# Optimization experiments

Measured on AMD Instinct MI355X. Metric: run time of the kernel, lower is better.

## Reference

```python
import jax, jax.numpy as jnp
import numpy as np

N_LEVELS = 16
NFPL = 2
LOG2_T = 19
TABLE_SIZE = 1 << LOG2_T
BASE_RES = 16.0
FINEST_RES = 512.0
N_POINTS = 1048576

# hash primes from HashNeRF's hash() (xor of coord*prime per axis)
PRIMES = jnp.array([1, 2654435761, 805459861], dtype=jnp.uint32)
# corner offsets: index = 4*i + 2*j + k (i outermost), matching BOX_OFFSETS
OFFSETS = jnp.array([[i, j, k] for i in (0, 1) for j in (0, 1) for k in (0, 1)], dtype=jnp.int32)  # [8,3]


def setup_inputs() -> dict:
    key = jax.random.key(0)
    k1, k2 = jax.random.split(key)
    x = jax.random.uniform(k1, (N_POINTS, 3), dtype=jnp.float32)  # points in [0,1)^3
    # nn.Embedding tables init uniform(-1e-4, 1e-4), stacked over levels
    tables = jax.random.uniform(k2, (N_LEVELS, TABLE_SIZE, NFPL), minval=-1e-4, maxval=1e-4, dtype=jnp.float32)
    return {"x": x, "tables": tables}


def _level_embed(x, table, resolution):
    # x: [N,3] in box [0,1]^3; table: [T,F]; resolution: scalar float
    grid = 1.0 / resolution
    xc = jnp.clip(x, 0.0, 1.0)
    bl = jnp.floor(xc / grid).astype(jnp.int32)            # [N,3] bottom-left voxel idx
    vmin = bl.astype(jnp.float32) * grid                    # voxel_min_vertex
    vmax = vmin + grid                                      # voxel_max_vertex
    corners = bl[:, None, :] + OFFSETS[None, :, :]          # [N,8,3]
    h = corners.astype(jnp.uint32) * PRIMES                 # wrap-around uint32 mult
    idx = (h[..., 0] ^ h[..., 1] ^ h[..., 2]) & jnp.uint32(TABLE_SIZE - 1)  # [N,8]
    emb = table[idx.astype(jnp.int32)]                      # [N,8,F] gather
    # trilinear interp (weights use unclamped x as in the original)
    w = (x - vmin) / (vmax - vmin)                          # [N,3]
    w0, w1, w2 = w[:, 0:1], w[:, 1:2], w[:, 2:3]
    c00 = emb[:, 0] * (1 - w0) + emb[:, 4] * w0
    c01 = emb[:, 1] * (1 - w0) + emb[:, 5] * w0
    c10 = emb[:, 2] * (1 - w0) + emb[:, 6] * w0
    c11 = emb[:, 3] * (1 - w0) + emb[:, 7] * w0
    c0 = c00 * (1 - w1) + c10 * w1
    c1 = c01 * (1 - w1) + c11 * w1
    return c0 * (1 - w2) + c1 * w2                          # [N,F]


def reference(x, tables):
    b = np.exp((np.log(FINEST_RES) - np.log(BASE_RES)) / (N_LEVELS - 1))
    res = jnp.floor(BASE_RES * (b ** jnp.arange(N_LEVELS, dtype=jnp.float32)))  # [L]
    feats = jax.vmap(_level_embed, in_axes=(None, 0, 0))(x, tables, res)        # [L,N,F]
    out = jnp.moveaxis(feats, 0, 1).reshape(x.shape[0], N_LEVELS * NFPL)        # [N,32]
    # original: if last dim != 16, F.pad(x, (0, 16 - D)); negative pad crops
    D = out.shape[-1]
    if D > 16:
        out = out[:, :16]
    elif D < 16:
        out = jnp.pad(out, ((0, 0), (0, 16 - D)))
    return out
```

## Files before the change

kernel.cpp:

```cpp
#include <hip/hip_runtime.h>
#include <hip/hip_fp16.h>
#include <stdint.h>


#define TABLE_SIZE (1u << 19)
#define TMASK (TABLE_SIZE - 1u)
#define P2 2654435761u
#define P3 805459861u

#define FSCALE 8192.0f
#define FINV   1.220703125e-4f

#define QUAD_BYTES_OFF 262144
#define PAIR_BYTES_OFF 16777216

#define OFF_Q3 0
#define OFF_Q4 33792
#define OFF_Q5 99392
#define OFF_Q6 226892

__device__ __forceinline__ uint32_t pack_s(float a, float b) {
    __half2 h = __floats2half2_rn(a * FSCALE, b * FSCALE);
    return *(uint32_t*)&h;
}
__device__ __forceinline__ uint32_t pack_r(float a, float b) {
    __half2 h = __floats2half2_rn(a, b);
    return *(uint32_t*)&h;
}
__device__ __forceinline__ float2 h2f(uint32_t u) {
    __half2 h = *(__half2*)&u;
    return __half22float2(h);
}
__device__ __forceinline__ uint32_t getc(const uint4 v, int k) {
    return k == 0 ? v.x : k == 1 ? v.y : k == 2 ? v.z : v.w;
}

__global__ __launch_bounds__(256) void build_tables_kernel(
    const float* __restrict__ tables, float2* __restrict__ dense,
    uint4* __restrict__ quads, uint2* __restrict__ pairs)
{
    const int role = (int)blockIdx.y;
    const int e = (int)blockIdx.x * 256 + (int)threadIdx.x;

    if (role < 4) {
        int DK, offq, l = 3 + role;
        switch (role) {
            case 0: DK = 32; offq = OFF_Q3; break;
            case 1: DK = 40; offq = OFF_Q4; break;
            case 2: DK = 50; offq = OFF_Q5; break;
            default:DK = 64; offq = OFF_Q6; break;
        }
        const int E = (DK + 1) * DK * DK;
        if (e >= E) return;
        const int d2 = DK * DK;
        const int i = e / d2;
        const int rem = e - i * d2;
        const int j = rem / DK;
        const int k = rem - j * DK;
        const float2* __restrict__ tab = (const float2*)tables + (size_t)l * (size_t)TABLE_SIZE;
        const uint32_t hx  = (uint32_t)i;
        const uint32_t hy0 = (uint32_t)j * P2, hy1 = hy0 + P2;
        const uint32_t hz0 = (uint32_t)k * P3, hz1 = hz0 + P3;
        const float2 v00 = tab[(hx ^ hy0 ^ hz0) & TMASK];
        const float2 v01 = tab[(hx ^ hy0 ^ hz1) & TMASK];
        const float2 v10 = tab[(hx ^ hy1 ^ hz0) & TMASK];
        const float2 v11 = tab[(hx ^ hy1 ^ hz1) & TMASK];
        uint4 u;
        u.x = pack_s(v00.x, v00.y);
        u.y = pack_s(v01.x, v01.y);
        u.z = pack_s(v10.x, v10.y);
        u.w = pack_s(v11.x, v11.y);
        quads[offq + e] = u;
    } else if (role == 4) {
        const int E = 81 * 81 * 80;
        if (e >= E) return;
        const int i = e / 6480;
        const int rem = e - i * 6480;
        const int j = rem / 80;
        const int k = rem - j * 80;
        const float2* __restrict__ tab = (const float2*)tables + (size_t)7 * (size_t)TABLE_SIZE;
        const uint32_t hb = (uint32_t)i ^ ((uint32_t)j * P2);
        const float2 a = tab[(hb ^ ((uint32_t)k * P3)) & TMASK];
        const float2 b = tab[(hb ^ ((uint32_t)(k + 1) * P3)) & TMASK];
        uint2 u;
        u.x = pack_s(a.x, a.y);
        u.y = pack_s(b.x, b.y);
        pairs[e] = u;
    } else {
        if (e >= 31750) return;
        int lv, DIM, off;
        if (e < 4913)       { lv = 0; DIM = 17; off = 0; }
        else if (e < 14174) { lv = 1; DIM = 21; off = 4913; }
        else                { lv = 2; DIM = 26; off = 14174; }
        const int le = e - off;
        const int d2 = DIM * DIM;
        const int i = le / d2;
        const int rem = le - i * d2;
        const int j = rem / DIM;
        const int k = rem - j * DIM;
        const uint32_t h = ((uint32_t)i ^ ((uint32_t)j * P2) ^ ((uint32_t)k * P3)) & TMASK;
        const float2* __restrict__ tab = (const float2*)tables + (size_t)lv * (size_t)TABLE_SIZE;
        dense[e] = tab[h];
    }
}

struct PQ {
    uint4 qa[4], qb[4];
    float wx[4], wy[4], wz[4];
};
struct PP {
    uint2 d00[4], d01[4], d10[4], d11[4];
    float wx[4], wy[4], wz[4];
};

template<int DK>
__device__ __forceinline__ void q_issue(const uint4* __restrict__ tab,
        const float px[4], const float py[4], const float pz[4], PQ& s)
{
    const float R = (float)DK, g = 1.0f / R;
    const int d2 = DK * DK;
#pragma unroll
    for (int k = 0; k < 4; ++k) {
        const float cx = fminf(fmaxf(px[k], 0.0f), 1.0f);
        const float cy = fminf(fmaxf(py[k], 0.0f), 1.0f);
        const float cz = fminf(fmaxf(pz[k], 0.0f), 1.0f);
        const int bx = min((int)floorf(cx * R), DK - 1);
        const int by = min((int)floorf(cy * R), DK - 1);
        const int bz = min((int)floorf(cz * R), DK - 1);
        s.wx[k] = (px[k] - (float)bx * g) * R;
        s.wy[k] = (py[k] - (float)by * g) * R;
        s.wz[k] = (pz[k] - (float)bz * g) * R;
        const int ia = (bx * DK + by) * DK + bz;
        s.qa[k] = tab[ia];
        s.qb[k] = tab[ia + d2];
    }
}

__device__ __forceinline__ uint4 q_finish(const PQ& s)
{
    uint32_t r[4];
#pragma unroll
    for (int k = 0; k < 4; ++k) {
        const float wx = s.wx[k], wy = s.wy[k], wz = s.wz[k];
        const float omx = 1.0f - wx, omy = 1.0f - wy, omz = 1.0f - wz;
        const float2 a00 = h2f(s.qa[k].x), a01 = h2f(s.qa[k].y);
        const float2 a10 = h2f(s.qa[k].z), a11 = h2f(s.qa[k].w);
        const float2 b00 = h2f(s.qb[k].x), b01 = h2f(s.qb[k].y);
        const float2 b10 = h2f(s.qb[k].z), b11 = h2f(s.qb[k].w);
        const float m00a = a00.x*omx + b00.x*wx, m00b = a00.y*omx + b00.y*wx;
        const float m01a = a01.x*omx + b01.x*wx, m01b = a01.y*omx + b01.y*wx;
        const float m10a = a10.x*omx + b10.x*wx, m10b = a10.y*omx + b10.y*wx;
        const float m11a = a11.x*omx + b11.x*wx, m11b = a11.y*omx + b11.y*wx;
        const float c0a = m00a*omz + m01a*wz, c0b = m00b*omz + m01b*wz;
        const float c1a = m10a*omz + m11a*wz, c1b = m10b*omz + m11b*wz;
        r[k] = pack_r(c0a*omy + c1a*wy, c0b*omy + c1b*wy);
    }
    return make_uint4(r[0], r[1], r[2], r[3]);
}

__device__ __forceinline__ void p_issue(const uint2* __restrict__ pairs,
        const float px[4], const float py[4], const float pz[4], PP& s)
{
    const float R = 80.f, g = 1.0f / R;
#pragma unroll
    for (int k = 0; k < 4; ++k) {
        const float cx = fminf(fmaxf(px[k], 0.0f), 1.0f);
        const float cy = fminf(fmaxf(py[k], 0.0f), 1.0f);
        const float cz = fminf(fmaxf(pz[k], 0.0f), 1.0f);
        const int bx = min((int)floorf(cx * R), 79);
        const int by = min((int)floorf(cy * R), 79);
        const int bz = min((int)floorf(cz * R), 79);
        s.wx[k] = (px[k] - (float)bx * g) * R;
        s.wy[k] = (py[k] - (float)by * g) * R;
        s.wz[k] = (pz[k] - (float)bz * g) * R;
        const int ix = (bx * 81 + by) * 80 + bz;
        s.d00[k] = pairs[ix];
        s.d01[k] = pairs[ix + 80];
        s.d10[k] = pairs[ix + 6480];
        s.d11[k] = pairs[ix + 6560];
    }
}

__device__ __forceinline__ uint4 p_finish(const PP& s)
{
    uint32_t r[4];
#pragma unroll
    for (int k = 0; k < 4; ++k) {
        const float wx = s.wx[k], wy = s.wy[k], wz = s.wz[k];
        const float omx = 1.0f - wx, omy = 1.0f - wy, omz = 1.0f - wz;
        const float2 a00 = h2f(s.d00[k].x), z00 = h2f(s.d00[k].y);
        const float2 a01 = h2f(s.d01[k].x), z01 = h2f(s.d01[k].y);
        const float2 a10 = h2f(s.d10[k].x), z10 = h2f(s.d10[k].y);
        const float2 a11 = h2f(s.d11[k].x), z11 = h2f(s.d11[k].y);
        const float c00a = a00.x*omz + z00.x*wz, c00b = a00.y*omz + z00.y*wz;
        const float c01a = a01.x*omz + z01.x*wz, c01b = a01.y*omz + z01.y*wz;
        const float c10a = a10.x*omz + z10.x*wz, c10b = a10.y*omz + z10.y*wz;
        const float c11a = a11.x*omz + z11.x*wz, c11b = a11.y*omz + z11.y*wz;
        const float e0a = c00a*omy + c01a*wy, e0b = c00b*omy + c01b*wy;
        const float e1a = c10a*omy + c11a*wy, e1b = c10b*omy + c11b*wy;
        r[k] = pack_r(e0a*omx + e1a*wx, e0b*omx + e1b*wx);
    }
    return make_uint4(r[0], r[1], r[2], r[3]);
}

__device__ __forceinline__ void store4(uint32_t* __restrict__ wsh,
        size_t lofs, int p0, int n, uint4 r)
{
    if (p0 + 4 <= n) {
        *(uint4*)(wsh + lofs + p0) = r;
    } else {
#pragma unroll
        for (int k = 0; k < 4; ++k)
            if (p0 + k < n) wsh[lofs + p0 + k] = getc(r, k);
    }
}

__global__ __launch_bounds__(256) void embed_grouped_kernel(
    const float* __restrict__ x, const uint4* __restrict__ quads,
    const uint2* __restrict__ pairs, uint32_t* __restrict__ wsh,
    int n, int bpl)
{
    const int bid = (int)blockIdx.x;
    const int grp = bid / bpl;
    const int pb = bid - grp * bpl;
    const int p0 = pb * 1024 + 4 * (int)threadIdx.x;
    if (p0 >= n) return;

    float px[4], py[4], pz[4];
    if (p0 + 4 <= n) {
        const float4* __restrict__ xv = (const float4*)(x + (size_t)3 * p0);
        const float4 f0 = xv[0], f1 = xv[1], f2 = xv[2];
        px[0] = f0.x; py[0] = f0.y; pz[0] = f0.z;
        px[1] = f0.w; py[1] = f1.x; pz[1] = f1.y;
        px[2] = f1.z; py[2] = f1.w; pz[2] = f2.x;
        px[3] = f2.y; py[3] = f2.z; pz[3] = f2.w;
    } else {
#pragma unroll
        for (int k = 0; k < 4; ++k) {
            const int i = min(p0 + k, n - 1);
            px[k] = x[3*i]; py[k] = x[3*i+1]; pz[k] = x[3*i+2];
        }
    }

    if (grp == 0) {
        PQ s3, s4, s5;
        q_issue<32>(quads + OFF_Q3, px, py, pz, s3);
        q_issue<40>(quads + OFF_Q4, px, py, pz, s4);
        store4(wsh, (size_t)3 * n, p0, n, q_finish(s3));
        q_issue<50>(quads + OFF_Q5, px, py, pz, s5);
        store4(wsh, (size_t)4 * n, p0, n, q_finish(s4));
        store4(wsh, (size_t)5 * n, p0, n, q_finish(s5));
    } else if (grp == 1) {
        PQ s6;
        q_issue<64>(quads + OFF_Q6, px, py, pz, s6);
        store4(wsh, (size_t)6 * n, p0, n, q_finish(s6));
    } else {
        PP s7;
        p_issue(pairs, px, py, pz, s7);
        store4(wsh, (size_t)7 * n, p0, n, p_finish(s7));
    }
}

__global__ __launch_bounds__(1024) void embed_lds_kernel(
    const float* __restrict__ x, const float2* __restrict__ dense,
    uint32_t* __restrict__ wsh, int n, int lv, int DIM, int E, int doff)
{
    extern __shared__ float2 lds[];
    for (int e = (int)threadIdx.x; e < E; e += 1024) lds[e] = dense[doff + e];
    __syncthreads();

    const int p0 = ((int)blockIdx.x * 1024 + (int)threadIdx.x) * 4;
    if (p0 >= n) return;

    const float R = (lv == 0) ? 16.f : (lv == 1) ? 20.f : 25.f;
    const float g = 1.0f / R;
    const int D2 = DIM * DIM;
    const int bmax = DIM - 2;

    float px[4], py[4], pz[4];
    if (p0 + 4 <= n) {
        const float4* __restrict__ xv = (const float4*)(x + (size_t)3 * p0);
        const float4 f0 = xv[0], f1 = xv[1], f2 = xv[2];
        px[0] = f0.x; py[0] = f0.y; pz[0] = f0.z;
        px[1] = f0.w; py[1] = f1.x; pz[1] = f1.y;
        px[2] = f1.z; py[2] = f1.w; pz[2] = f2.x;
        px[3] = f2.y; py[3] = f2.z; pz[3] = f2.w;
    } else {
#pragma unroll
        for (int k = 0; k < 4; ++k) {
            const int i = min(p0 + k, n - 1);
            px[k] = x[3*i]; py[k] = x[3*i+1]; pz[k] = x[3*i+2];
        }
    }

    uint32_t r[4];
#pragma unroll
    for (int k = 0; k < 4; ++k) {
        const float cx = fminf(fmaxf(px[k], 0.0f), 1.0f);
        const float cy = fminf(fmaxf(py[k], 0.0f), 1.0f);
        const float cz = fminf(fmaxf(pz[k], 0.0f), 1.0f);
        const int bx = min((int)floorf(cx * R), bmax);
        const int by = min((int)floorf(cy * R), bmax);
        const int bz = min((int)floorf(cz * R), bmax);
        const float wx = (px[k] - (float)bx * g) * R;
        const float wy = (py[k] - (float)by * g) * R;
        const float wz = (pz[k] - (float)bz * g) * R;
        const int c = (bx * DIM + by) * DIM + bz;
        const float2 e000 = lds[c];
        const float2 e001 = lds[c + 1];
        const float2 e010 = lds[c + DIM];
        const float2 e011 = lds[c + DIM + 1];
        const float2 e100 = lds[c + D2];
        const float2 e101 = lds[c + D2 + 1];
        const float2 e110 = lds[c + D2 + DIM];
        const float2 e111 = lds[c + D2 + DIM + 1];
        const float omx = 1.0f - wx, omy = 1.0f - wy, omz = 1.0f - wz;
        const float c00a = e000.x*omx + e100.x*wx, c00b = e000.y*omx + e100.y*wx;
        const float c01a = e001.x*omx + e101.x*wx, c01b = e001.y*omx + e101.y*wx;
        const float c10a = e010.x*omx + e110.x*wx, c10b = e010.y*omx + e110.y*wx;
        const float c11a = e011.x*omx + e111.x*wx, c11b = e011.y*omx + e111.y*wx;
        const float c0a = c00a*omy + c10a*wy, c0b = c00b*omy + c10b*wy;
        const float c1a = c01a*omy + c11a*wy, c1b = c01b*omy + c11b*wy;
        r[k] = pack_s(c0a*omz + c1a*wz, c0b*omz + c1b*wz);
    }
    store4(wsh, (size_t)lv * n, p0, n, make_uint4(r[0], r[1], r[2], r[3]));
}

__global__ __launch_bounds__(256) void aos_kernel(
    const uint32_t* __restrict__ wsh, float* __restrict__ out, int n)
{
    const int p0 = ((int)blockIdx.x * 256 + (int)threadIdx.x) * 4;
    if (p0 >= n) return;

    if (p0 + 4 <= n) {
        const uint4 v0 = *(const uint4*)(wsh + 0 * (size_t)n + p0);
        const uint4 v1 = *(const uint4*)(wsh + 1 * (size_t)n + p0);
        const uint4 v2 = *(const uint4*)(wsh + 2 * (size_t)n + p0);
        const uint4 v3 = *(const uint4*)(wsh + 3 * (size_t)n + p0);
        const uint4 v4 = *(const uint4*)(wsh + 4 * (size_t)n + p0);
        const uint4 v5 = *(const uint4*)(wsh + 5 * (size_t)n + p0);
        const uint4 v6 = *(const uint4*)(wsh + 6 * (size_t)n + p0);
        const uint4 v7 = *(const uint4*)(wsh + 7 * (size_t)n + p0);
#pragma unroll
        for (int k = 0; k < 4; ++k) {
            const float2 f0 = h2f(getc(v0, k)), f1 = h2f(getc(v1, k));
            const float2 f2 = h2f(getc(v2, k)), f3 = h2f(getc(v3, k));
            const float2 f4 = h2f(getc(v4, k)), f5 = h2f(getc(v5, k));
            const float2 f6 = h2f(getc(v6, k)), f7 = h2f(getc(v7, k));
            float4* __restrict__ op = (float4*)(out + (size_t)(p0 + k) * 16);
            op[0] = make_float4(f0.x*FINV, f0.y*FINV, f1.x*FINV, f1.y*FINV);
            op[1] = make_float4(f2.x*FINV, f2.y*FINV, f3.x*FINV, f3.y*FINV);
            op[2] = make_float4(f4.x*FINV, f4.y*FINV, f5.x*FINV, f5.y*FINV);
            op[3] = make_float4(f6.x*FINV, f6.y*FINV, f7.x*FINV, f7.y*FINV);
        }
    } else {
        for (int k = 0; k < 4 && p0 + k < n; ++k) {
            const int i = p0 + k;
            float* __restrict__ op = out + (size_t)i * 16;
#pragma unroll
            for (int l = 0; l < 8; ++l) {
                const float2 f = h2f(wsh[(size_t)l * n + i]);
                op[2*l + 0] = f.x * FINV;
                op[2*l + 1] = f.y * FINV;
            }
        }
    }
}

__global__ __launch_bounds__(256) void hash_embed_mono_kernel(
    const float* __restrict__ x, const float* __restrict__ tables,
    float* __restrict__ out, int n)
{
    const int i = blockIdx.x * 256 + threadIdx.x;
    if (i >= n) return;
    const float px = x[3*i+0], py = x[3*i+1], pz = x[3*i+2];
    const float cx = fminf(fmaxf(px, 0.0f), 1.0f);
    const float cy = fminf(fmaxf(py, 0.0f), 1.0f);
    const float cz = fminf(fmaxf(pz, 0.0f), 1.0f);
    const float resf[8] = {16.f,20.f,25.f,32.f,40.f,50.f,64.f,80.f};
    float o[16];
#pragma unroll
    for (int l = 0; l < 8; ++l) {
        const float R = resf[l], g = 1.0f / R;
        const int bx = (int)floorf(cx*R), by = (int)floorf(cy*R), bz = (int)floorf(cz*R);
        const float wx = (px - bx*g)*R, wy = (py - by*g)*R, wz = (pz - bz*g)*R;
        const uint32_t hx0 = (uint32_t)bx, hx1 = hx0+1u;
        const uint32_t hy0 = (uint32_t)by*P2, hy1 = hy0+P2;
        const uint32_t hz0 = (uint32_t)bz*P3, hz1 = hz0+P3;
        const float2* tab = (const float2*)(tables) + (size_t)l*(size_t)TABLE_SIZE;
        const float2 e000 = tab[(hx0^hy0^hz0)&TMASK], e001 = tab[(hx0^hy0^hz1)&TMASK];
        const float2 e010 = tab[(hx0^hy1^hz0)&TMASK], e011 = tab[(hx0^hy1^hz1)&TMASK];
        const float2 e100 = tab[(hx1^hy0^hz0)&TMASK], e101 = tab[(hx1^hy0^hz1)&TMASK];
        const float2 e110 = tab[(hx1^hy1^hz0)&TMASK], e111 = tab[(hx1^hy1^hz1)&TMASK];
        const float omx = 1.f-wx, omy = 1.f-wy, omz = 1.f-wz;
        const float c00a = e000.x*omx + e100.x*wx, c00b = e000.y*omx + e100.y*wx;
        const float c01a = e001.x*omx + e101.x*wx, c01b = e001.y*omx + e101.y*wx;
        const float c10a = e010.x*omx + e110.x*wx, c10b = e010.y*omx + e110.y*wx;
        const float c11a = e011.x*omx + e111.x*wx, c11b = e011.y*omx + e111.y*wx;
        const float c0a = c00a*omy + c10a*wy, c0b = c00b*omy + c10b*wy;
        const float c1a = c01a*omy + c11a*wy, c1b = c01b*omy + c11b*wy;
        o[2*l+0] = c0a*omz + c1a*wz;
        o[2*l+1] = c0b*omz + c1b*wz;
    }
    float4* op = (float4*)(out + (size_t)i * 16);
    op[0] = make_float4(o[0],o[1],o[2],o[3]);
    op[1] = make_float4(o[4],o[5],o[6],o[7]);
    op[2] = make_float4(o[8],o[9],o[10],o[11]);
    op[3] = make_float4(o[12],o[13],o[14],o[15]);
}

extern "C" void kernel_launch(void* const* d_in, const int* in_sizes, int n_in,
                              void* d_out, int out_size, void* d_ws, size_t ws_size,
                              hipStream_t stream) {
    const float* x = (const float*)d_in[0];
    const float* tables = (const float*)d_in[1];
    float* out = (float*)d_out;
    const int n = in_sizes[0] / 3;

    static int cap = -1;
    if (cap < 0) {
        cap = (hipFuncSetAttribute((const void*)embed_lds_kernel,
                  hipFuncAttributeMaxDynamicSharedMemorySize, 140608) == hipSuccess)
              ? 1 : 0;
    }
    const size_t ws_needed = (size_t)8 * (size_t)n * sizeof(uint32_t);
    if (ws_size < ws_needed || cap == 0) {
        hash_embed_mono_kernel<<<(n + 255) / 256, 256, 0, stream>>>(x, tables, out, n);
        return;
    }

    uint32_t* wsh = (uint32_t*)d_ws;
    float2* dense = (float2*)out;
    uint4*  quads = (uint4*)((char*)out + QUAD_BYTES_OFF);
    uint2*  pairs = (uint2*)((char*)out + PAIR_BYTES_OFF);

    build_tables_kernel<<<dim3(2051, 6), 256, 0, stream>>>(tables, dense, quads, pairs);

    static const int DIMt[3] = {17, 21, 26};
    static const int Et[3]   = {4913, 9261, 17576};
    static const int OFFt[3] = {0, 4913, 14174};
    const int lgrid = (n + 4095) / 4096;
    for (int lv = 0; lv < 3; ++lv) {
        embed_lds_kernel<<<lgrid, 1024, (size_t)Et[lv] * sizeof(float2), stream>>>(
            x, dense, wsh, n, lv, DIMt[lv], Et[lv], OFFt[lv]);
    }

    const int bpl = (n + 1023) / 1024;
    embed_grouped_kernel<<<3 * bpl, 256, 0, stream>>>(x, quads, pairs, wsh, n, bpl);

    aos_kernel<<<(n + 1023) / 1024, 256, 0, stream>>>(wsh, out, n);
}
```

Before: 255.6 us.

## Fuse dense coarse levels into output kernel with fp16 LDS table

Measured after the change: 217.1 us. 1.18x faster.

```diff
diff --git a/kernel.cpp b/kernel.cpp
--- a/kernel.cpp
+++ b/kernel.cpp
@@ -19,6 +19,11 @@
 #define OFF_Q5 99392
 #define OFF_Q6 226892
 
+#define DENSE_L1_OFF 4913
+#define DENSE_L2_OFF 14174
+#define DENSE_E 31750
+#define DENSE_BYTES (DENSE_E * 4)
+
 __device__ __forceinline__ uint32_t pack_s(float a, float b) {
     __half2 h = __floats2half2_rn(a * FSCALE, b * FSCALE);
     return *(uint32_t*)&h;
@@ -35,21 +40,26 @@
     return k == 0 ? v.x : k == 1 ? v.y : k == 2 ? v.z : v.w;
 }
 
+__device__ __forceinline__ void quad_geom(int l, float& R, int& DK, int& offq) {
+    switch (l) {
+        case 3: R=32.f; DK=32; offq=OFF_Q3; break;
+        case 4: R=40.f; DK=40; offq=OFF_Q4; break;
+        case 5: R=50.f; DK=50; offq=OFF_Q5; break;
+        default:R=64.f; DK=64; offq=OFF_Q6; break;
+    }
+}
+
 __global__ __launch_bounds__(256) void build_tables_kernel(
-    const float* __restrict__ tables, float2* __restrict__ dense,
+    const float* __restrict__ tables, uint32_t* __restrict__ dense,
     uint4* __restrict__ quads, uint2* __restrict__ pairs)
 {
     const int role = (int)blockIdx.y;
     const int e = (int)blockIdx.x * 256 + (int)threadIdx.x;
 
     if (role < 4) {
-        int DK, offq, l = 3 + role;
-        switch (role) {
-            case 0: DK = 32; offq = OFF_Q3; break;
-            case 1: DK = 40; offq = OFF_Q4; break;
-            case 2: DK = 50; offq = OFF_Q5; break;
-            default:DK = 64; offq = OFF_Q6; break;
-        }
+        float Rf; int DK, offq;
+        quad_geom(3 + role, Rf, DK, offq);
+        const int l = 3 + role;
         const int E = (DK + 1) * DK * DK;
         if (e >= E) return;
         const int d2 = DK * DK;
@@ -87,11 +97,11 @@
         u.y = pack_s(b.x, b.y);
         pairs[e] = u;
     } else {
-        if (e >= 31750) return;
+        if (e >= DENSE_E) return;
         int lv, DIM, off;
-        if (e < 4913)       { lv = 0; DIM = 17; off = 0; }
-        else if (e < 14174) { lv = 1; DIM = 21; off = 4913; }
-        else                { lv = 2; DIM = 26; off = 14174; }
+        if (e < DENSE_L1_OFF)      { lv = 0; DIM = 17; off = 0; }
+        else if (e < DENSE_L2_OFF) { lv = 1; DIM = 21; off = DENSE_L1_OFF; }
+        else                       { lv = 2; DIM = 26; off = DENSE_L2_OFF; }
         const int le = e - off;
         const int d2 = DIM * DIM;
         const int i = le / d2;
@@ -100,25 +110,20 @@
         const int k = rem - j * DIM;
         const uint32_t h = ((uint32_t)i ^ ((uint32_t)j * P2) ^ ((uint32_t)k * P3)) & TMASK;
         const float2* __restrict__ tab = (const float2*)tables + (size_t)lv * (size_t)TABLE_SIZE;
-        dense[e] = tab[h];
-    }
-}
-
-struct PQ {
+        const float2 v = tab[h];
+        dense[e] = pack_s(v.x, v.y);
+    }
+}
+
+template<int DK>
+__device__ __forceinline__ uint4 embed_quad4(const uint4* __restrict__ tab,
+        const float px[4], const float py[4], const float pz[4])
+{
+    const float R = (float)DK;
+    const float g = 1.0f / R;
+    const int d2 = DK * DK;
     uint4 qa[4], qb[4];
     float wx[4], wy[4], wz[4];
-};
-struct PP {
-    uint2 d00[4], d01[4], d10[4], d11[4];
-    float wx[4], wy[4], wz[4];
-};
-
-template<int DK>
-__device__ __forceinline__ void q_issue(const uint4* __restrict__ tab,
-        const float px[4], const float py[4], const float pz[4], PQ& s)
-{
-    const float R = (float)DK, g = 1.0f / R;
-    const int d2 = DK * DK;
 #pragma unroll
     for (int k = 0; k < 4; ++k) {
         const float cx = fminf(fmaxf(px[k], 0.0f), 1.0f);
@@ -127,41 +132,38 @@
         const int bx = min((int)floorf(cx * R), DK - 1);
         const int by = min((int)floorf(cy * R), DK - 1);
         const int bz = min((int)floorf(cz * R), DK - 1);
-        s.wx[k] = (px[k] - (float)bx * g) * R;
-        s.wy[k] = (py[k] - (float)by * g) * R;
-        s.wz[k] = (pz[k] - (float)bz * g) * R;
+        wx[k] = (px[k] - (float)bx * g) * R;
+        wy[k] = (py[k] - (float)by * g) * R;
+        wz[k] = (pz[k] - (float)bz * g) * R;
         const int ia = (bx * DK + by) * DK + bz;
-        s.qa[k] = tab[ia];
-        s.qb[k] = tab[ia + d2];
-    }
-}
-
-__device__ __forceinline__ uint4 q_finish(const PQ& s)
-{
+        qa[k] = tab[ia];
+        qb[k] = tab[ia + d2];
+    }
     uint32_t r[4];
 #pragma unroll
     for (int k = 0; k < 4; ++k) {
-        const float wx = s.wx[k], wy = s.wy[k], wz = s.wz[k];
-        const float omx = 1.0f - wx, omy = 1.0f - wy, omz = 1.0f - wz;
-        const float2 a00 = h2f(s.qa[k].x), a01 = h2f(s.qa[k].y);
-        const float2 a10 = h2f(s.qa[k].z), a11 = h2f(s.qa[k].w);
-        const float2 b00 = h2f(s.qb[k].x), b01 = h2f(s.qb[k].y);
-        const float2 b10 = h2f(s.qb[k].z), b11 = h2f(s.qb[k].w);
-        const float m00a = a00.x*omx + b00.x*wx, m00b = a00.y*omx + b00.y*wx;
-        const float m01a = a01.x*omx + b01.x*wx, m01b = a01.y*omx + b01.y*wx;
-        const float m10a = a10.x*omx + b10.x*wx, m10b = a10.y*omx + b10.y*wx;
-        const float m11a = a11.x*omx + b11.x*wx, m11b = a11.y*omx + b11.y*wx;
-        const float c0a = m00a*omz + m01a*wz, c0b = m00b*omz + m01b*wz;
-        const float c1a = m10a*omz + m11a*wz, c1b = m10b*omz + m11b*wz;
-        r[k] = pack_r(c0a*omy + c1a*wy, c0b*omy + c1b*wy);
+        const float omx = 1.0f - wx[k], omy = 1.0f - wy[k], omz = 1.0f - wz[k];
+        const float2 a00 = h2f(qa[k].x), a01 = h2f(qa[k].y);
+        const float2 a10 = h2f(qa[k].z), a11 = h2f(qa[k].w);
+        const float2 b00 = h2f(qb[k].x), b01 = h2f(qb[k].y);
+        const float2 b10 = h2f(qb[k].z), b11 = h2f(qb[k].w);
+        const float m00a = a00.x*omx + b00.x*wx[k], m00b = a00.y*omx + b00.y*wx[k];
+        const float m01a = a01.x*omx + b01.x*wx[k], m01b = a01.y*omx + b01.y*wx[k];
+        const float m10a = a10.x*omx + b10.x*wx[k], m10b = a10.y*omx + b10.y*wx[k];
+        const float m11a = a11.x*omx + b11.x*wx[k], m11b = a11.y*omx + b11.y*wx[k];
+        const float c0a = m00a*omz + m01a*wz[k], c0b = m00b*omz + m01b*wz[k];
+        const float c1a = m10a*omz + m11a*wz[k], c1b = m10b*omz + m11b*wz[k];
+        r[k] = pack_r(c0a*omy + c1a*wy[k], c0b*omy + c1b*wy[k]);
     }
     return make_uint4(r[0], r[1], r[2], r[3]);
 }
 
-__device__ __forceinline__ void p_issue(const uint2* __restrict__ pairs,
-        const float px[4], const float py[4], const float pz[4], PP& s)
+__device__ __forceinline__ uint4 embed_pair4(const uint2* __restrict__ pairs,
+        const float px[4], const float py[4], const float pz[4])
 {
     const float R = 80.f, g = 1.0f / R;
+    uint2 d00[4], d01[4], d10[4], d11[4];
+    float wx[4], wy[4], wz[4];
 #pragma unroll
     for (int k = 0; k < 4; ++k) {
         const float cx = fminf(fmaxf(px[k], 0.0f), 1.0f);
@@ -170,52 +172,35 @@
         const int bx = min((int)floorf(cx * R), 79);
         const int by = min((int)floorf(cy * R), 79);
         const int bz = min((int)floorf(cz * R), 79);
-        s.wx[k] = (px[k] - (float)bx * g) * R;
-        s.wy[k] = (py[k] - (float)by * g) * R;
-        s.wz[k] = (pz[k] - (float)bz * g) * R;
+        wx[k] = (px[k] - (float)bx * g) * R;
+        wy[k] = (py[k] - (float)by * g) * R;
+        wz[k] = (pz[k] - (float)bz * g) * R;
         const int ix = (bx * 81 + by) * 80 + bz;
-        s.d00[k] = pairs[ix];
-        s.d01[k] = pairs[ix + 80];
-        s.d10[k] = pairs[ix + 6480];
-        s.d11[k] = pairs[ix + 6560];
-    }
-}
-
-__device__ __forceinline__ uint4 p_finish(const PP& s)
-{
+        d00[k] = pairs[ix];
+        d01[k] = pairs[ix + 80];
+        d10[k] = pairs[ix + 6480];
+        d11[k] = pairs[ix + 6560];
+    }
     uint32_t r[4];
 #pragma unroll
     for (int k = 0; k < 4; ++k) {
-        const float wx = s.wx[k], wy = s.wy[k], wz = s.wz[k];
-        const float omx = 1.0f - wx, omy = 1.0f - wy, omz = 1.0f - wz;
-        const float2 a00 = h2f(s.d00[k].x), z00 = h2f(s.d00[k].y);
-        const float2 a01 = h2f(s.d01[k].x), z01 = h2f(s.d01[k].y);
-        const float2 a10 = h2f(s.d10[k].x), z10 = h2f(s.d10[k].y);
-        const float2 a11 = h2f(s.d11[k].x), z11 = h2f(s.d11[k].y);
-        const float c00a = a00.x*omz + z00.x*wz, c00b = a00.y*omz + z00.y*wz;
-        const float c01a = a01.x*omz + z01.x*wz, c01b = a01.y*omz + z01.y*wz;
-        const float c10a = a10.x*omz + z10.x*wz, c10b = a10.y*omz + z10.y*wz;
-        const float c11a = a11.x*omz + z11.x*wz, c11b = a11.y*omz + z11.y*wz;
-        const float e0a = c00a*omy + c01a*wy, e0b = c00b*omy + c01b*wy;
-        const float e1a = c10a*omy + c11a*wy, e1b = c10b*omy + c11b*wy;
-        r[k] = pack_r(e0a*omx + e1a*wx, e0b*omx + e1b*wx);
+        const float omx = 1.0f - wx[k], omy = 1.0f - wy[k], omz = 1.0f - wz[k];
+        const float2 a00 = h2f(d00[k].x), z00 = h2f(d00[k].y);
+        const float2 a01 = h2f(d01[k].x), z01 = h2f(d01[k].y);
+        const float2 a10 = h2f(d10[k].x), z10 = h2f(d10[k].y);
+        const float2 a11 = h2f(d11[k].x), z11 = h2f(d11[k].y);
+        const float c00a = a00.x*omz + z00.x*wz[k], c00b = a00.y*omz + z00.y*wz[k];
+        const float c01a = a01.x*omz + z01.x*wz[k], c01b = a01.y*omz + z01.y*wz[k];
+        const float c10a = a10.x*omz + z10.x*wz[k], c10b = a10.y*omz + z10.y*wz[k];
+        const float c11a = a11.x*omz + z11.x*wz[k], c11b = a11.y*omz + z11.y*wz[k];
+        const float e0a = c00a*omy + c01a*wy[k], e0b = c00b*omy + c01b*wy[k];
+        const float e1a = c10a*omy + c11a*wy[k], e1b = c10b*omy + c11b*wy[k];
+        r[k] = pack_r(e0a*omx + e1a*wx[k], e0b*omx + e1b*wx[k]);
     }
     return make_uint4(r[0], r[1], r[2], r[3]);
 }
 
-__device__ __forceinline__ void store4(uint32_t* __restrict__ wsh,
-        size_t lofs, int p0, int n, uint4 r)
-{
-    if (p0 + 4 <= n) {
-        *(uint4*)(wsh + lofs + p0) = r;
-    } else {
-#pragma unroll
-        for (int k = 0; k < 4; ++k)
-            if (p0 + k < n) wsh[lofs + p0 + k] = getc(r, k);
-    }
-}
-
-__global__ __launch_bounds__(256) void embed_grouped_kernel(
+__global__ __launch_bounds__(256, 4) void embed_levels_kernel(
     const float* __restrict__ x, const uint4* __restrict__ quads,
     const uint2* __restrict__ pairs, uint32_t* __restrict__ wsh,
     int n, int bpl)
@@ -242,40 +227,40 @@
         }
     }
 
+    const int nstore = min(4, n - p0);
+
+#define STORE_ROW(l, r) { \
+    uint32_t* __restrict__ wl = wsh + (size_t)(l) * (size_t)n; \
+    if (nstore == 4) *(uint4*)(wl + p0) = (r); \
+    else for (int k = 0; k < nstore; ++k) wl[p0 + k] = getc((r), k); }
+
     if (grp == 0) {
-        PQ s3, s4, s5;
-        q_issue<32>(quads + OFF_Q3, px, py, pz, s3);
-        q_issue<40>(quads + OFF_Q4, px, py, pz, s4);
-        store4(wsh, (size_t)3 * n, p0, n, q_finish(s3));
-        q_issue<50>(quads + OFF_Q5, px, py, pz, s5);
-        store4(wsh, (size_t)4 * n, p0, n, q_finish(s4));
-        store4(wsh, (size_t)5 * n, p0, n, q_finish(s5));
+        const uint4 r3 = embed_quad4<32>(quads + OFF_Q3, px, py, pz);
+        STORE_ROW(3, r3)
+        const uint4 r4 = embed_quad4<40>(quads + OFF_Q4, px, py, pz);
+        STORE_ROW(4, r4)
     } else if (grp == 1) {
-        PQ s6;
-        q_issue<64>(quads + OFF_Q6, px, py, pz, s6);
-        store4(wsh, (size_t)6 * n, p0, n, q_finish(s6));
+        const uint4 r5 = embed_quad4<50>(quads + OFF_Q5, px, py, pz);
+        STORE_ROW(5, r5)
+    } else if (grp == 2) {
+        const uint4 r6 = embed_quad4<64>(quads + OFF_Q6, px, py, pz);
+        STORE_ROW(6, r6)
     } else {
-        PP s7;
-        p_issue(pairs, px, py, pz, s7);
-        store4(wsh, (size_t)7 * n, p0, n, p_finish(s7));
-    }
-}
-
-__global__ __launch_bounds__(1024) void embed_lds_kernel(
-    const float* __restrict__ x, const float2* __restrict__ dense,
-    uint32_t* __restrict__ wsh, int n, int lv, int DIM, int E, int doff)
-{
-    extern __shared__ float2 lds[];
-    for (int e = (int)threadIdx.x; e < E; e += 1024) lds[e] = dense[doff + e];
+        const uint4 r7 = embed_pair4(pairs, px, py, pz);
+        STORE_ROW(7, r7)
+    }
+}
+
+__global__ __launch_bounds__(1024) void final_kernel(
+    const float* __restrict__ x, const uint32_t* wsh,
+    float* __restrict__ out, int n)
+{
+    extern __shared__ uint32_t lds[];
+    for (int e = (int)threadIdx.x; e < DENSE_E; e += 1024) lds[e] = wsh[e];
     __syncthreads();
 
     const int p0 = ((int)blockIdx.x * 1024 + (int)threadIdx.x) * 4;
     if (p0 >= n) return;
-
-    const float R = (lv == 0) ? 16.f : (lv == 1) ? 20.f : 25.f;
-    const float g = 1.0f / R;
-    const int D2 = DIM * DIM;
-    const int bmax = DIM - 2;
 
     float px[4], py[4], pz[4];
     if (p0 + 4 <= n) {
@@ -293,77 +278,75 @@
         }
     }
 
-    uint32_t r[4];
-#pragma unroll
-    for (int k = 0; k < 4; ++k) {
-        const float cx = fminf(fmaxf(px[k], 0.0f), 1.0f);
-        const float cy = fminf(fmaxf(py[k], 0.0f), 1.0f);
-        const float cz = fminf(fmaxf(pz[k], 0.0f), 1.0f);
-        const int bx = min((int)floorf(cx * R), bmax);
-        const int by = min((int)floorf(cy * R), bmax);
-        const int bz = min((int)floorf(cz * R), bmax);
-        const float wx = (px[k] - (float)bx * g) * R;
-        const float wy = (py[k] - (float)by * g) * R;
-        const float wz = (pz[k] - (float)bz * g) * R;
-        const int c = (bx * DIM + by) * DIM + bz;
-        const float2 e000 = lds[c];
-        const float2 e001 = lds[c + 1];
-        const float2 e010 = lds[c + DIM];
-        const float2 e011 = lds[c + DIM + 1];
-        const float2 e100 = lds[c + D2];
-        const float2 e101 = lds[c + D2 + 1];
-        const float2 e110 = lds[c + D2 + DIM];
-        const float2 e111 = lds[c + D2 + DIM + 1];
-        const float omx = 1.0f - wx, omy = 1.0f - wy, omz = 1.0f - wz;
-        const float c00a = e000.x*omx + e100.x*wx, c00b = e000.y*omx + e100.y*wx;
-        const float c01a = e001.x*omx + e101.x*wx, c01b = e001.y*omx + e101.y*wx;
-        const float c10a = e010.x*omx + e110.x*wx, c10b = e010.y*omx + e110.y*wx;
-        const float c11a = e011.x*omx + e111.x*wx, c11b = e011.y*omx + e111.y*wx;
-        const float c0a = c00a*omy + c10a*wy, c0b = c00b*omy + c10b*wy;
-        const float c1a = c01a*omy + c11a*wy, c1b = c01b*omy + c11b*wy;
-        r[k] = pack_s(c0a*omz + c1a*wz, c0b*omz + c1b*wz);
-    }
-    store4(wsh, (size_t)lv * n, p0, n, make_uint4(r[0], r[1], r[2], r[3]));
-}
-
-__global__ __launch_bounds__(256) void aos_kernel(
-    const uint32_t* __restrict__ wsh, float* __restrict__ out, int n)
-{
-    const int p0 = ((int)blockIdx.x * 256 + (int)threadIdx.x) * 4;
-    if (p0 >= n) return;
-
+    uint4 v[5];
     if (p0 + 4 <= n) {
-        const uint4 v0 = *(const uint4*)(wsh + 0 * (size_t)n + p0);
-        const uint4 v1 = *(const uint4*)(wsh + 1 * (size_t)n + p0);
-        const uint4 v2 = *(const uint4*)(wsh + 2 * (size_t)n + p0);
-        const uint4 v3 = *(const uint4*)(wsh + 3 * (size_t)n + p0);
-        const uint4 v4 = *(const uint4*)(wsh + 4 * (size_t)n + p0);
-        const uint4 v5 = *(const uint4*)(wsh + 5 * (size_t)n + p0);
-        const uint4 v6 = *(const uint4*)(wsh + 6 * (size_t)n + p0);
-        const uint4 v7 = *(const uint4*)(wsh + 7 * (size_t)n + p0);
-#pragma unroll
-        for (int k = 0; k < 4; ++k) {
-            const float2 f0 = h2f(getc(v0, k)), f1 = h2f(getc(v1, k));
-            const float2 f2 = h2f(getc(v2, k)), f3 = h2f(getc(v3, k));
-            const float2 f4 = h2f(getc(v4, k)), f5 = h2f(getc(v5, k));
-            const float2 f6 = h2f(getc(v6, k)), f7 = h2f(getc(v7, k));
-            float4* __restrict__ op = (float4*)(out + (size_t)(p0 + k) * 16);
-            op[0] = make_float4(f0.x*FINV, f0.y*FINV, f1.x*FINV, f1.y*FINV);
-            op[1] = make_float4(f2.x*FINV, f2.y*FINV, f3.x*FINV, f3.y*FINV);
-            op[2] = make_float4(f4.x*FINV, f4.y*FINV, f5.x*FINV, f5.y*FINV);
-            op[3] = make_float4(f6.x*FINV, f6.y*FINV, f7.x*FINV, f7.y*FINV);
+#pragma unroll
+        for (int l = 0; l < 5; ++l)
+            v[l] = *(const uint4*)(wsh + (size_t)(l + 3) * n + p0);
+    } else {
+#pragma unroll
+        for (int l = 0; l < 5; ++l) {
+            uint4 t;
+            t.x = wsh[(size_t)(l+3)*n + min(p0+0, n-1)];
+            t.y = wsh[(size_t)(l+3)*n + min(p0+1, n-1)];
+            t.z = wsh[(size_t)(l+3)*n + min(p0+2, n-1)];
+            t.w = wsh[(size_t)(l+3)*n + min(p0+3, n-1)];
+            v[l] = t;
         }
-    } else {
-        for (int k = 0; k < 4 && p0 + k < n; ++k) {
-            const int i = p0 + k;
-            float* __restrict__ op = out + (size_t)i * 16;
-#pragma unroll
-            for (int l = 0; l < 8; ++l) {
-                const float2 f = h2f(wsh[(size_t)l * n + i]);
-                op[2*l + 0] = f.x * FINV;
-                op[2*l + 1] = f.y * FINV;
-            }
+    }
+
+    float la[3][4], lb[3][4];
+#pragma unroll
+    for (int k = 0; k < 4; ++k) {
+#pragma unroll
+        for (int lv = 0; lv < 3; ++lv) {
+            const float R  = (lv == 0) ? 16.f : (lv == 1) ? 20.f : 25.f;
+            const int DIM  = (lv == 0) ? 17 : (lv == 1) ? 21 : 26;
+            const int off  = (lv == 0) ? 0 : (lv == 1) ? DENSE_L1_OFF : DENSE_L2_OFF;
+            const float g = 1.0f / R;
+            const int D2 = DIM * DIM;
+            const int bmax = DIM - 2;
+            const float cx = fminf(fmaxf(px[k], 0.0f), 1.0f);
+            const float cy = fminf(fmaxf(py[k], 0.0f), 1.0f);
+            const float cz = fminf(fmaxf(pz[k], 0.0f), 1.0f);
+            const int bx = min((int)floorf(cx * R), bmax);
+            const int by = min((int)floorf(cy * R), bmax);
+            const int bz = min((int)floorf(cz * R), bmax);
+            const float wx = (px[k] - (float)bx * g) * R;
+            const float wy = (py[k] - (float)by * g) * R;
+            const float wz = (pz[k] - (float)bz * g) * R;
+            const int c = off + (bx * DIM + by) * DIM + bz;
+            const float2 e000 = h2f(lds[c]);
+            const float2 e001 = h2f(lds[c + 1]);
+            const float2 e010 = h2f(lds[c + DIM]);
+            const float2 e011 = h2f(lds[c + DIM + 1]);
+            const float2 e100 = h2f(lds[c + D2]);
+            const float2 e101 = h2f(lds[c + D2 + 1]);
+            const float2 e110 = h2f(lds[c + D2 + DIM]);
+            const float2 e111 = h2f(lds[c + D2 + DIM + 1]);
+            const float omx = 1.0f - wx, omy = 1.0f - wy, omz = 1.0f - wz;
+            const float c00a = e000.x*omx + e100.x*wx, c00b = e000.y*omx + e100.y*wx;
+            const float c01a = e001.x*omx + e101.x*wx, c01b = e001.y*omx + e101.y*wx;
+            const float c10a = e010.x*omx + e110.x*wx, c10b = e010.y*omx + e110.y*wx;
+            const float c11a = e011.x*omx + e111.x*wx, c11b = e011.y*omx + e111.y*wx;
+            const float c0a = c00a*omy + c10a*wy, c0b = c00b*omy + c10b*wy;
+            const float c1a = c01a*omy + c11a*wy, c1b = c01b*omy + c11b*wy;
+            la[lv][k] = c0a*omz + c1a*wz;
+            lb[lv][k] = c0b*omz + c1b*wz;
         }
+    }
+
+#pragma unroll
+    for (int k = 0; k < 4; ++k) {
+        if (p0 + k >= n) break;
+        const float2 f3v = h2f(getc(v[0], k)), f4v = h2f(getc(v[1], k));
+        const float2 f5v = h2f(getc(v[2], k)), f6v = h2f(getc(v[3], k));
+        const float2 f7v = h2f(getc(v[4], k));
+        float4* __restrict__ op = (float4*)(out + (size_t)(p0 + k) * 16);
+        op[0] = make_float4(la[0][k]*FINV, lb[0][k]*FINV, la[1][k]*FINV, lb[1][k]*FINV);
+        op[1] = make_float4(la[2][k]*FINV, lb[2][k]*FINV, f3v.x*FINV, f3v.y*FINV);
+        op[2] = make_float4(f4v.x*FINV, f4v.y*FINV, f5v.x*FINV, f5v.y*FINV);
+        op[3] = make_float4(f6v.x*FINV, f6v.y*FINV, f7v.x*FINV, f7v.y*FINV);
     }
 }
 
@@ -419,8 +402,8 @@
 
     static int cap = -1;
     if (cap < 0) {
-        cap = (hipFuncSetAttribute((const void*)embed_lds_kernel,
-                  hipFuncAttributeMaxDynamicSharedMemorySize, 140608) == hipSuccess)
+        cap = (hipFuncSetAttribute((const void*)final_kernel,
+                  hipFuncAttributeMaxDynamicSharedMemorySize, DENSE_BYTES) == hipSuccess)
               ? 1 : 0;
     }
     const size_t ws_needed = (size_t)8 * (size_t)n * sizeof(uint32_t);
@@ -430,23 +413,14 @@
     }
 
     uint32_t* wsh = (uint32_t*)d_ws;
-    float2* dense = (float2*)out;
+    uint32_t* dense = (uint32_t*)d_ws;
     uint4*  quads = (uint4*)((char*)out + QUAD_BYTES_OFF);
     uint2*  pairs = (uint2*)((char*)out + PAIR_BYTES_OFF);
 
     build_tables_kernel<<<dim3(2051, 6), 256, 0, stream>>>(tables, dense, quads, pairs);
 
-    static const int DIMt[3] = {17, 21, 26};
-    static const int Et[3]   = {4913, 9261, 17576};
-    static const int OFFt[3] = {0, 4913, 14174};
-    const int lgrid = (n + 4095) / 4096;
-    for (int lv = 0; lv < 3; ++lv) {
-        embed_lds_kernel<<<lgrid, 1024, (size_t)Et[lv] * sizeof(float2), stream>>>(
-            x, dense, wsh, n, lv, DIMt[lv], Et[lv], OFFt[lv]);
-    }
-
     const int bpl = (n + 1023) / 1024;
-    embed_grouped_kernel<<<3 * bpl, 256, 0, stream>>>(x, quads, pairs, wsh, n, bpl);
-
-    aos_kernel<<<(n + 1023) / 1024, 256, 0, stream>>>(wsh, out, n);
-}
+    embed_levels_kernel<<<4 * bpl, 256, 0, stream>>>(x, quads, pairs, wsh, n, bpl);
+
+    final_kernel<<<(n + 4095) / 4096, 1024, DENSE_BYTES, stream>>>(x, wsh, out, n);
+}
```
